# Performance work log

Measured on AMD Instinct MI355X. Metric: run time of the kernel, lower is better.

## Reference

```python
import jax, jax.numpy as jnp
import numpy as np

N_NODES = 40000


def _gcn_conv(x, edge_index, W, b):
    """PyG GCNConv: add self-loops, symmetric degree normalization,
    linear transform, gather-scale-scatter aggregation, bias."""
    n = x.shape[0]
    loops = jnp.arange(n, dtype=edge_index.dtype)
    src = jnp.concatenate([edge_index[0], loops])  # [E+N]
    dst = jnp.concatenate([edge_index[1], loops])  # [E+N]
    ones = jnp.ones(src.shape[0], dtype=x.dtype)
    deg = jax.ops.segment_sum(ones, dst, num_segments=n)  # in-degree incl. self-loop
    dinv = jnp.where(deg > 0, jax.lax.rsqrt(deg), 0.0)
    norm = dinv[src] * dinv[dst]  # [E+N]
    h = x @ W  # [n, out]
    msg = h[src] * norm[:, None]  # [E+N, out] gather + scale
    out = jax.ops.segment_sum(msg, dst, num_segments=n)  # scatter-add
    return out + b


def setup_inputs() -> dict:
    key = jax.random.key(0)
    k = jax.random.split(key, 6)
    n, din, dh, dout = N_NODES, 128, 128, 64
    x = jax.random.normal(k[0], (n, din), dtype=jnp.float32)
    edge_index = jax.random.randint(k[1], (2, 640000), 0, n, dtype=jnp.int64)
    W1 = jax.random.normal(k[2], (din, dh), dtype=jnp.float32) / np.sqrt(din)
    b1 = jnp.zeros((dh,), dtype=jnp.float32)
    W2 = jax.random.normal(k[3], (dh, dout), dtype=jnp.float32) / np.sqrt(dh)
    b2 = jnp.zeros((dout,), dtype=jnp.float32)
    return {"x": x, "edge_index": edge_index, "W1": W1, "b1": b1, "W2": W2, "b2": b2}


def reference(x, edge_index, W1, b1, W2, b2):
    h = jax.nn.relu(_gcn_conv(x, edge_index, W1, b1))
    return _gcn_conv(h, edge_index, W2, b2)
```

## Files before the change

kernel.cpp:

```cpp
#include <hip/hip_runtime.h>
#include <hip/hip_fp16.h>


#define N_NODES 40000
#define DIN 128
#define DH 128
#define DOUT 64
#define NEDGES 640000
#define CAP 64

typedef _Float16 f16x8 __attribute__((ext_vector_type(8)));
typedef float f32x4 __attribute__((ext_vector_type(4)));

__global__ void k_init(int* __restrict__ deg, const float* __restrict__ W1,
                       const float* __restrict__ W2,
                       _Float16* __restrict__ WT1, _Float16* __restrict__ WT2, int n) {
    int i = blockIdx.x * 256 + threadIdx.x;
    if (i < n) deg[i] = 0;
    if (i < DIN * DH) {
        int k = i >> 7, nn = i & 127;
        WT1[(size_t)nn * DIN + k] = (_Float16)W1[i];
    }
    if (i < DH * DOUT) {
        int k = i >> 6, nn = i & 63;
        WT2[(size_t)nn * DH + k] = (_Float16)W2[i];
    }
}

__global__ __launch_bounds__(256) void k_work1(
    const float* __restrict__ x, const _Float16* __restrict__ WT,
    __half* __restrict__ h,
    const int4* __restrict__ src4, const int4* __restrict__ dst4,
    int* __restrict__ deg, int* __restrict__ ssrc)
{
    if (blockIdx.x < 625) {
        const int wave = blockIdx.x * 4 + (threadIdx.x >> 6);
        const int lane = threadIdx.x & 63;
        const int m = lane & 15, quad = lane >> 4;

        f32x4 acc[8];
#pragma unroll
        for (int nt = 0; nt < 8; ++nt) acc[nt] = (f32x4){0.f, 0.f, 0.f, 0.f};

        const float* xrow = x + (size_t)(wave * 16 + m) * DIN + quad * 8;
#pragma unroll
        for (int ks = 0; ks < 4; ++ks) {
            float4 xa = *(const float4*)(xrow + ks * 32);
            float4 xb = *(const float4*)(xrow + ks * 32 + 4);
            f16x8 a = { (_Float16)xa.x, (_Float16)xa.y, (_Float16)xa.z, (_Float16)xa.w,
                        (_Float16)xb.x, (_Float16)xb.y, (_Float16)xb.z, (_Float16)xb.w };
#pragma unroll
            for (int nt = 0; nt < 8; ++nt) {
                f16x8 b = *(const f16x8*)(WT + (size_t)(nt * 16 + m) * DIN + ks * 32 + quad * 8);
                acc[nt] = __builtin_amdgcn_mfma_f32_16x16x32_f16(a, b, acc[nt], 0, 0, 0);
            }
        }
#pragma unroll
        for (int r = 0; r < 4; ++r) {
            int orow = wave * 16 + quad * 4 + r;
#pragma unroll
            for (int nt = 0; nt < 8; ++nt)
                h[(size_t)orow * DH + nt * 16 + m] = (__half)acc[nt][r];
        }
    } else {
        int e = (blockIdx.x - 625) * 256 + threadIdx.x;
        if (e < NEDGES / 4) {
            int4 s = src4[e];
            int4 d = dst4[e];
            int p0 = atomicAdd(&deg[d.x], 1); if (p0 < CAP) ssrc[d.x * CAP + p0] = s.x;
            int p1 = atomicAdd(&deg[d.y], 1); if (p1 < CAP) ssrc[d.y * CAP + p1] = s.y;
            int p2 = atomicAdd(&deg[d.z], 1); if (p2 < CAP) ssrc[d.z * CAP + p2] = s.z;
            int p3 = atomicAdd(&deg[d.w], 1); if (p3 < CAP) ssrc[d.w * CAP + p3] = s.w;
        }
    }
}

__global__ __launch_bounds__(256) void k_agg1g2(
    const int* __restrict__ deg, const int* __restrict__ ssrc,
    const __half* __restrict__ h1, const float* __restrict__ b1,
    const _Float16* __restrict__ WT2, __half* __restrict__ h2)
{
    __shared__ _Float16 xs[16][136];
    const int w = threadIdx.x >> 6;
    const int lane = threadIdx.x & 63;
    const int node0 = blockIdx.x * 16;
    const __half2* hp = (const __half2*)h1;

    for (int i = 0; i < 4; ++i) {
        const int node = node0 + w * 4 + i;
        const int dg = deg[node];
        const int cnt = min(dg, CAP);
        const float dn = rsqrtf((float)(dg + 1));
        float2 self = __half22float2(hp[(size_t)node * 64 + lane]);
        float2 acc = { self.x * dn, self.y * dn };
        int sv = (lane < cnt) ? ssrc[node * CAP + lane] : 0;
        float dval = (lane < cnt) ? rsqrtf((float)(deg[sv] + 1)) : 0.f;
        int e = 0;
        for (; e + 4 <= cnt; e += 4) {
            int s0 = __shfl(sv, e),     s1 = __shfl(sv, e + 1);
            int s2 = __shfl(sv, e + 2), s3 = __shfl(sv, e + 3);
            float w0 = __shfl(dval, e),     w1 = __shfl(dval, e + 1);
            float w2 = __shfl(dval, e + 2), w3 = __shfl(dval, e + 3);
            float2 v0 = __half22float2(hp[(size_t)s0 * 64 + lane]);
            float2 v1 = __half22float2(hp[(size_t)s1 * 64 + lane]);
            float2 v2 = __half22float2(hp[(size_t)s2 * 64 + lane]);
            float2 v3 = __half22float2(hp[(size_t)s3 * 64 + lane]);
            acc.x += (v0.x * w0 + v1.x * w1) + (v2.x * w2 + v3.x * w3);
            acc.y += (v0.y * w0 + v1.y * w1) + (v2.y * w2 + v3.y * w3);
        }
        for (; e < cnt; ++e) {
            int s = __shfl(sv, e);
            float wv = __shfl(dval, e);
            float2 v = __half22float2(hp[(size_t)s * 64 + lane]);
            acc.x += v.x * wv; acc.y += v.y * wv;
        }
        float vx = dn * acc.x + b1[2 * lane];
        float vy = dn * acc.y + b1[2 * lane + 1];
        xs[w * 4 + i][2 * lane]     = (_Float16)(vx > 0.f ? vx : 0.f);
        xs[w * 4 + i][2 * lane + 1] = (_Float16)(vy > 0.f ? vy : 0.f);
    }
    __syncthreads();

    const int m = lane & 15, quad = lane >> 4;
    f32x4 acc2 = (f32x4){0.f, 0.f, 0.f, 0.f};
#pragma unroll
    for (int ks = 0; ks < 4; ++ks) {
        f16x8 a = *(const f16x8*)&xs[m][ks * 32 + quad * 8];
        f16x8 b = *(const f16x8*)(WT2 + (size_t)(w * 16 + m) * DH + ks * 32 + quad * 8);
        acc2 = __builtin_amdgcn_mfma_f32_16x16x32_f16(a, b, acc2, 0, 0, 0);
    }
#pragma unroll
    for (int r = 0; r < 4; ++r) {
        int nrow = node0 + quad * 4 + r;
        float dn = rsqrtf((float)(deg[nrow] + 1));
        h2[(size_t)nrow * DOUT + w * 16 + m] = (__half)(acc2[r] * dn);
    }
}

__global__ __launch_bounds__(256) void k_agg2(
    const int* __restrict__ deg, const int* __restrict__ ssrc,
    const __half* __restrict__ h, const float* __restrict__ b2,
    float* __restrict__ out)
{
    const int node = blockIdx.x * 4 + (threadIdx.x >> 6);
    const int lane = threadIdx.x & 63;
    const int dg = deg[node];
    const int cnt = min(dg, CAP);
    float acc = (float)h[(size_t)node * 64 + lane];
    int sv = (lane < cnt) ? ssrc[node * CAP + lane] : 0;
    int e = 0;
    for (; e + 8 <= cnt; e += 8) {
        int s0 = __shfl(sv, e),     s1 = __shfl(sv, e + 1);
        int s2 = __shfl(sv, e + 2), s3 = __shfl(sv, e + 3);
        int s4 = __shfl(sv, e + 4), s5 = __shfl(sv, e + 5);
        int s6 = __shfl(sv, e + 6), s7 = __shfl(sv, e + 7);
        float v0 = (float)h[(size_t)s0 * 64 + lane];
        float v1 = (float)h[(size_t)s1 * 64 + lane];
        float v2 = (float)h[(size_t)s2 * 64 + lane];
        float v3 = (float)h[(size_t)s3 * 64 + lane];
        float v4 = (float)h[(size_t)s4 * 64 + lane];
        float v5 = (float)h[(size_t)s5 * 64 + lane];
        float v6 = (float)h[(size_t)s6 * 64 + lane];
        float v7 = (float)h[(size_t)s7 * 64 + lane];
        acc += ((v0 + v1) + (v2 + v3)) + ((v4 + v5) + (v6 + v7));
    }
    for (; e < cnt; ++e) {
        int s = __shfl(sv, e);
        acc += (float)h[(size_t)s * 64 + lane];
    }
    out[(size_t)node * 64 + lane] = rsqrtf((float)(dg + 1)) * acc + b2[lane];
}

extern "C" void kernel_launch(void* const* d_in, const int* in_sizes, int n_in,
                              void* d_out, int out_size, void* d_ws, size_t ws_size,
                              hipStream_t stream) {
    const float* x  = (const float*)d_in[0];
    const int*   ei = (const int*)d_in[1];
    const float* W1 = (const float*)d_in[2];
    const float* b1 = (const float*)d_in[3];
    const float* W2 = (const float*)d_in[4];
    const float* b2 = (const float*)d_in[5];
    float* out = (float*)d_out;

    const int n = N_NODES, E = NEDGES;
    const int* src = ei;
    const int* dst = ei + E;

    char* ws = (char*)d_ws;
    int*      deg  = (int*)(ws + 0);
    _Float16* WT1  = (_Float16*)(ws + 163840);
    _Float16* WT2  = (_Float16*)(ws + 196608);
    int*      ssrc = (int*)(ws + 212992);
    __half*   h1   = (__half*)(ws + 10452992);
    __half*   h2   = (__half*)(ws + 20692992);

    k_init   <<<(n + 255) / 256, 256, 0, stream>>>(deg, W1, W2, WT1, WT2, n);
    k_work1  <<<1250, 256, 0, stream>>>(x, WT1, h1, (const int4*)src, (const int4*)dst,
                                        deg, ssrc);
    k_agg1g2 <<<n / 16, 256, 0, stream>>>(deg, ssrc, h1, b1, WT2, h2);
    k_agg2   <<<n / 4,  256, 0, stream>>>(deg, ssrc, h2, b2, out);
}
```

Baseline: 181.4 us.

## Partition edge bucketing by XCD node range and store neighbor ids as 16-bit

Edge-insertion blocks are now assigned so that each group of blocks (by blockIdx mod 8) only handles destination nodes in one 5000-node range. The intent is for the atomics and ssrc writes to stay within one XCD's L2. Each edge chunk is re-read by all eight groups, which multiplies edge index traffic. The neighbor list is stored as unsigned short to halve its footprint and gather traffic. Edge blocks are now scheduled before the GEMM blocks.

Result: faster. 170.8 us (-5.9%).

```diff
diff --git a/kernel.cpp b/kernel.cpp
--- a/kernel.cpp
+++ b/kernel.cpp
@@ -8,6 +8,9 @@
 #define DOUT 64
 #define NEDGES 640000
 #define CAP 64
+#define NBUCKET 640
+#define I4_PER_CHUNK 2000
+#define NODES_PER_XCD 5000
 
 typedef _Float16 f16x8 __attribute__((ext_vector_type(8)));
 typedef float f32x4 __attribute__((ext_vector_type(4)));
@@ -31,10 +34,35 @@
     const float* __restrict__ x, const _Float16* __restrict__ WT,
     __half* __restrict__ h,
     const int4* __restrict__ src4, const int4* __restrict__ dst4,
-    int* __restrict__ deg, int* __restrict__ ssrc)
+    int* __restrict__ deg, unsigned short* __restrict__ ssrc)
 {
-    if (blockIdx.x < 625) {
-        const int wave = blockIdx.x * 4 + (threadIdx.x >> 6);
+    if (blockIdx.x < NBUCKET) {
+        const int xg = blockIdx.x & 7;
+        const int c  = blockIdx.x >> 3;
+        const int lo = xg * NODES_PER_XCD, hi = lo + NODES_PER_XCD;
+        const int e0 = c * I4_PER_CHUNK, e1 = e0 + I4_PER_CHUNK;
+        for (int e = e0 + threadIdx.x; e < e1; e += 256) {
+            int4 d = dst4[e];
+            int4 s = src4[e];
+            if (d.x >= lo && d.x < hi) {
+                int p = atomicAdd(&deg[d.x], 1);
+                if (p < CAP) ssrc[d.x * CAP + p] = (unsigned short)s.x;
+            }
+            if (d.y >= lo && d.y < hi) {
+                int p = atomicAdd(&deg[d.y], 1);
+                if (p < CAP) ssrc[d.y * CAP + p] = (unsigned short)s.y;
+            }
+            if (d.z >= lo && d.z < hi) {
+                int p = atomicAdd(&deg[d.z], 1);
+                if (p < CAP) ssrc[d.z * CAP + p] = (unsigned short)s.z;
+            }
+            if (d.w >= lo && d.w < hi) {
+                int p = atomicAdd(&deg[d.w], 1);
+                if (p < CAP) ssrc[d.w * CAP + p] = (unsigned short)s.w;
+            }
+        }
+    } else {
+        const int wave = (blockIdx.x - NBUCKET) * 4 + (threadIdx.x >> 6);
         const int lane = threadIdx.x & 63;
         const int m = lane & 15, quad = lane >> 4;
 
@@ -62,21 +90,11 @@
             for (int nt = 0; nt < 8; ++nt)
                 h[(size_t)orow * DH + nt * 16 + m] = (__half)acc[nt][r];
         }
-    } else {
-        int e = (blockIdx.x - 625) * 256 + threadIdx.x;
-        if (e < NEDGES / 4) {
-            int4 s = src4[e];
-            int4 d = dst4[e];
-            int p0 = atomicAdd(&deg[d.x], 1); if (p0 < CAP) ssrc[d.x * CAP + p0] = s.x;
-            int p1 = atomicAdd(&deg[d.y], 1); if (p1 < CAP) ssrc[d.y * CAP + p1] = s.y;
-            int p2 = atomicAdd(&deg[d.z], 1); if (p2 < CAP) ssrc[d.z * CAP + p2] = s.z;
-            int p3 = atomicAdd(&deg[d.w], 1); if (p3 < CAP) ssrc[d.w * CAP + p3] = s.w;
-        }
     }
 }
 
 __global__ __launch_bounds__(256) void k_agg1g2(
-    const int* __restrict__ deg, const int* __restrict__ ssrc,
+    const int* __restrict__ deg, const unsigned short* __restrict__ ssrc,
     const __half* __restrict__ h1, const float* __restrict__ b1,
     const _Float16* __restrict__ WT2, __half* __restrict__ h2)
 {
@@ -93,7 +111,7 @@
         const float dn = rsqrtf((float)(dg + 1));
         float2 self = __half22float2(hp[(size_t)node * 64 + lane]);
         float2 acc = { self.x * dn, self.y * dn };
-        int sv = (lane < cnt) ? ssrc[node * CAP + lane] : 0;
+        int sv = (lane < cnt) ? (int)ssrc[node * CAP + lane] : 0;
         float dval = (lane < cnt) ? rsqrtf((float)(deg[sv] + 1)) : 0.f;
         int e = 0;
         for (; e + 4 <= cnt; e += 4) {
@@ -138,7 +156,7 @@
 }
 
 __global__ __launch_bounds__(256) void k_agg2(
-    const int* __restrict__ deg, const int* __restrict__ ssrc,
+    const int* __restrict__ deg, const unsigned short* __restrict__ ssrc,
     const __half* __restrict__ h, const float* __restrict__ b2,
     float* __restrict__ out)
 {
@@ -147,7 +165,7 @@
     const int dg = deg[node];
     const int cnt = min(dg, CAP);
     float acc = (float)h[(size_t)node * 64 + lane];
-    int sv = (lane < cnt) ? ssrc[node * CAP + lane] : 0;
+    int sv = (lane < cnt) ? (int)ssrc[node * CAP + lane] : 0;
     int e = 0;
     for (; e + 8 <= cnt; e += 8) {
         int s0 = __shfl(sv, e),     s1 = __shfl(sv, e + 1);
@@ -187,16 +205,16 @@
     const int* dst = ei + E;
 
     char* ws = (char*)d_ws;
-    int*      deg  = (int*)(ws + 0);
-    _Float16* WT1  = (_Float16*)(ws + 163840);
-    _Float16* WT2  = (_Float16*)(ws + 196608);
-    int*      ssrc = (int*)(ws + 212992);
-    __half*   h1   = (__half*)(ws + 10452992);
-    __half*   h2   = (__half*)(ws + 20692992);
+    int*            deg  = (int*)(ws + 0);
+    _Float16*       WT1  = (_Float16*)(ws + 163840);
+    _Float16*       WT2  = (_Float16*)(ws + 196608);
+    unsigned short* ssrc = (unsigned short*)(ws + 212992);
+    __half*         h1   = (__half*)(ws + 5332992);
+    __half*         h2   = (__half*)(ws + 15572992);
 
     k_init   <<<(n + 255) / 256, 256, 0, stream>>>(deg, W1, W2, WT1, WT2, n);
-    k_work1  <<<1250, 256, 0, stream>>>(x, WT1, h1, (const int4*)src, (const int4*)dst,
-                                        deg, ssrc);
+    k_work1  <<<NBUCKET + 625, 256, 0, stream>>>(x, WT1, h1, (const int4*)src,
+                                                 (const int4*)dst, deg, ssrc);
     k_agg1g2 <<<n / 16, 256, 0, stream>>>(deg, ssrc, h1, b1, WT2, h2);
     k_agg2   <<<n / 4,  256, 0, stream>>>(deg, ssrc, h2, b2, out);
 }
```
